# Kernel tuning notes

Hardware: AMD Instinct MI355X
Metric: run time of the kernel (lower is better)

## Reference

```python
import jax, jax.numpy as jnp
import numpy as np

IN_FEATURES = 4096
OUT_FEATURES = 4096
NUM_GROUPS = 32
HARDTANH_MIN = -2.0
HARDTANH_MAX = 2.0
EPS = 1e-6


def setup_inputs() -> dict:
    key = jax.random.key(0)
    k1, k2 = jax.random.split(key)
    x = jax.random.normal(k1, (8192, IN_FEATURES), dtype=jnp.float32)
    W = jax.random.normal(k2, (OUT_FEATURES, IN_FEATURES), dtype=jnp.float32)
    b = jnp.zeros((OUT_FEATURES,), dtype=jnp.float32)
    return {"x": x, "W": W, "b": b}


def reference(x, W, b):
    B = x.shape[0]
    group_size = OUT_FEATURES // NUM_GROUPS
    # GEMM: y[b, n] = sum_k x[b, k] * W[n, k]
    y = jnp.einsum("bk,nk->bn", x, W)
    # GroupNorm over each group of channels per row (no affine scale)
    yg = y.reshape(B, NUM_GROUPS, group_size)
    mean = jnp.mean(yg, axis=2, keepdims=True)
    var = jnp.mean((yg - mean) ** 2, axis=2, keepdims=True)
    norm = (yg - mean) / jnp.sqrt(var + EPS)
    norm = norm.reshape(B, OUT_FEATURES) + b[None, :]
    # kernel clamps to [-2, 2], then outer clamp to [hardtanh_min, hardtanh_max]
    out = jnp.clip(norm, -2.0, 2.0)
    out = jnp.clip(out, HARDTANH_MIN, HARDTANH_MAX)
    return out
```

## Files before the change

kernel.cpp:

```cpp
#include <hip/hip_runtime.h>
#include <hip/hip_bf16.h>
#include <stdint.h>

#define M_DIM 8192
#define N_DIM 4096
#define K_DIM 4096
#define BM 256
#define BN 256
#define BK 64
#define NT 64

typedef __attribute__((ext_vector_type(8))) short short8;
typedef __attribute__((ext_vector_type(4))) float f32x4;
typedef unsigned short ushort_t;

#define SBAR()  asm volatile("s_barrier" ::: "memory")
#define LGKM(n) asm volatile("s_waitcnt lgkmcnt(" #n ")" ::: "memory")
#define VM(n)   asm volatile("s_waitcnt vmcnt(" #n ")" ::: "memory")
#define SCHEDB() __builtin_amdgcn_sched_barrier(0)

__device__ __forceinline__ ushort_t f2bf(float f) {
    uint32_t u = __float_as_uint(f);
    uint32_t r = (u + 0x7FFFu + ((u >> 16) & 1u)) >> 16;
    return (ushort_t)r;
}

__global__ void cvt_f32_bf16(const float4* __restrict__ in, ushort* __restrict__ out4, int n4) {
    int i = blockIdx.x * blockDim.x + threadIdx.x;
    if (i < n4) {
        float4 v = in[i];
        ushort_t a = f2bf(v.x), b = f2bf(v.y), c = f2bf(v.z), d = f2bf(v.w);
        uint32_t lo = (uint32_t)a | ((uint32_t)b << 16);
        uint32_t hi = (uint32_t)c | ((uint32_t)d << 16);
        uint2* o = reinterpret_cast<uint2*>(out4);
        o[i] = make_uint2(lo, hi);
    }
}

__device__ __forceinline__ void gload_lds16(const ushort_t* g, void* l) {
    __builtin_amdgcn_global_load_lds(
        (const __attribute__((address_space(1))) unsigned int*)g,
        (__attribute__((address_space(3))) unsigned int*)l,
        16, 0, 0);
}

__global__ __launch_bounds__(256, 1)
void gemm_gn_kernel(const ushort_t* __restrict__ xb,
                    const ushort_t* __restrict__ wb,
                    const float*   __restrict__ bias,
                    float*         __restrict__ out)
{
    __shared__ char pool[131072];

    const int tid = threadIdx.x;
    const int w   = tid >> 6;
    const int l   = tid & 63;
    const int wr  = w >> 1;
    const int wc  = w & 1;
    const int l15 = l & 15;
    const int l4  = l >> 4;

    const int TN = N_DIM / BN;
    int bid = blockIdx.x;
    bid = (bid & 7) * 64 + (bid >> 3);
    const int brow = (bid / TN) * BM;
    const int bcol = (bid % TN) * BN;

    const int srow  = tid >> 3;
    const int sslot = (tid & 7) ^ (srow & 7);
    const ushort_t* gA = xb + (size_t)(brow + srow) * K_DIM + sslot * 8;
    const ushort_t* gB = wb + (size_t)(bcol + srow) * K_DIM + sslot * 8;
    const int wbase = w * 1024;

    auto STAGE_A = [&](int buf, int half, int kt) {
        const ushort_t* s = gA + (size_t)half * 128 * K_DIM + (size_t)kt * 64;
        char* d = pool + buf * 65536 + half * 16384 + wbase;
        gload_lds16(s,                      d);
        gload_lds16(s + (size_t)32 * K_DIM, d + 4096);
        gload_lds16(s + (size_t)64 * K_DIM, d + 8192);
        gload_lds16(s + (size_t)96 * K_DIM, d + 12288);
    };
    auto STAGE_B = [&](int buf, int half, int kt) {
        const ushort_t* s = gB + (size_t)half * 128 * K_DIM + (size_t)kt * 64;
        char* d = pool + buf * 65536 + 32768 + half * 16384 + wbase;
        gload_lds16(s,                      d);
        gload_lds16(s + (size_t)32 * K_DIM, d + 4096);
        gload_lds16(s + (size_t)64 * K_DIM, d + 8192);
        gload_lds16(s + (size_t)96 * K_DIM, d + 12288);
    };

    const int swz = (l15 & 7) << 4;
    const int x0  = (l4 * 16) ^ swz;
    const int x1  = (64 + l4 * 16) ^ swz;
    const int abase = (wr * 128 + l15) * 128;
    const int bbase = (wc * 128 + l15) * 128;

    short8 afL[8], afH[8], bfL[8], bfH[8];

    auto RD_A = [&](short8* dst, const char* Ab, int mi0) {
#pragma unroll
        for (int m = 0; m < 4; ++m) {
            dst[m * 2]     = *(const short8*)(Ab + abase + (mi0 + m) * 2048 + x0);
            dst[m * 2 + 1] = *(const short8*)(Ab + abase + (mi0 + m) * 2048 + x1);
        }
    };
    auto RD_B = [&](short8* dst, const char* Bb, int ni0) {
#pragma unroll
        for (int n = 0; n < 4; ++n) {
            dst[n * 2]     = *(const short8*)(Bb + bbase + (ni0 + n) * 2048 + x0);
            dst[n * 2 + 1] = *(const short8*)(Bb + bbase + (ni0 + n) * 2048 + x1);
        }
    };

    f32x4 acc[8][8];
#pragma unroll
    for (int i = 0; i < 8; ++i)
#pragma unroll
        for (int j = 0; j < 8; ++j) acc[i][j] = (f32x4){0.f, 0.f, 0.f, 0.f};

    auto MM = [&](short8* A, short8* B, int m0, int n0) {
#pragma unroll
        for (int k = 0; k < 2; ++k)
#pragma unroll
            for (int m = 0; m < 4; ++m)
#pragma unroll
                for (int n = 0; n < 4; ++n)
                    acc[m0 + m][n0 + n] = __builtin_amdgcn_mfma_f32_16x16x32_bf16(
                        A[m * 2 + k], B[n * 2 + k], acc[m0 + m][n0 + n], 0, 0, 0);
    };

    STAGE_A(0, 0, 0); STAGE_A(0, 1, 0);
    STAGE_B(0, 0, 0); STAGE_B(0, 1, 0);
    STAGE_B(1, 0, 1); STAGE_B(1, 1, 1);
    VM(8);
    SBAR();
    RD_B(bfL, pool + 32768, 0);
    RD_A(afL, pool, 0);

    for (int T = 0; T < NT; ++T) {
        const int cb = T & 1;
        const char* Ab = pool + cb * 65536;
        const char* Bb = Ab + 32768;
        const char* Abn = pool + (cb ^ 1) * 65536;
        const char* Bbn = Abn + 32768;

        SBAR();
        RD_A(afH, Ab, 4);
        if (T + 1 < NT) STAGE_A(cb ^ 1, 0, T + 1);
        LGKM(8);
        SCHEDB();
        __builtin_amdgcn_s_setprio(1);
        MM(afL, bfL, 0, 0);
        __builtin_amdgcn_s_setprio(0);

        SBAR();
        RD_B(bfH, Bb, 4);
        if (T + 1 < NT) STAGE_A(cb ^ 1, 1, T + 1);
        LGKM(8);
        SCHEDB();
        __builtin_amdgcn_s_setprio(1);
        MM(afH, bfL, 4, 0);
        __builtin_amdgcn_s_setprio(0);

        if (T + 2 < NT) STAGE_B(cb, 0, T + 2);
        LGKM(0);
        if (T < NT - 2) { VM(8); } else { VM(0); }
        SBAR();
        SCHEDB();
        if (T + 1 < NT) RD_B(bfL, Bbn, 0);
        __builtin_amdgcn_s_setprio(1);
        MM(afH, bfH, 4, 4);
        __builtin_amdgcn_s_setprio(0);

        if (T + 2 < NT) STAGE_B(cb, 1, T + 2);
        if (T < NT - 2) { VM(8); } else { VM(0); }
        SBAR();
        __builtin_amdgcn_s_setprio(1);
        MM(afL, bfH, 0, 4);
        __builtin_amdgcn_s_setprio(0);
        if (T + 1 < NT) RD_A(afL, Abn, 0);
    }

    float bv[8];
#pragma unroll
    for (int ni = 0; ni < 8; ++ni)
        bv[ni] = bias[bcol + wc * 128 + ni * 16 + l15];

    const float inv_gs = 1.0f / 128.0f;
#pragma unroll
    for (int mi = 0; mi < 8; ++mi) {
#pragma unroll
        for (int r = 0; r < 4; ++r) {
            float a = 0.f, b = 0.f;
#pragma unroll
            for (int ni = 0; ni < 8; ++ni) {
                float v = acc[mi][ni][r];
                a += v;
                b += v * v;
            }
#pragma unroll
            for (int m = 1; m < 16; m <<= 1) {
                a += __shfl_xor(a, m);
                b += __shfl_xor(b, m);
            }
            float mean = a * inv_gs;
            float var  = b * inv_gs - mean * mean;
            float inv  = rsqrtf(var + 1e-6f);
            int R = wr * 128 + mi * 16 + l4 * 4 + r;
            size_t rowbase = (size_t)(brow + R) * N_DIM + bcol + wc * 128 + l15;
#pragma unroll
            for (int ni = 0; ni < 8; ++ni) {
                float v = (acc[mi][ni][r] - mean) * inv + bv[ni];
                v = fminf(fmaxf(v, -2.0f), 2.0f);
                out[rowbase + ni * 16] = v;
            }
        }
    }
}

extern "C" void kernel_launch(void* const* d_in, const int* in_sizes, int n_in,
                              void* d_out, int out_size, void* d_ws, size_t ws_size,
                              hipStream_t stream) {
    const float* x = (const float*)d_in[0];
    const float* W = (const float*)d_in[1];
    const float* b = (const float*)d_in[2];
    float* out = (float*)d_out;

    ushort_t* xb = (ushort_t*)d_ws;
    ushort_t* wb = xb + (size_t)M_DIM * K_DIM;

    int n4x = M_DIM * K_DIM / 4;
    cvt_f32_bf16<<<(n4x + 255) / 256, 256, 0, stream>>>(
        (const float4*)x, xb, n4x);
    int n4w = N_DIM * K_DIM / 4;
    cvt_f32_bf16<<<(n4w + 255) / 256, 256, 0, stream>>>(
        (const float4*)W, wb, n4w);

    int grid = (M_DIM / BM) * (N_DIM / BN);
    gemm_gn_kernel<<<grid, 256, 0, stream>>>(xb, wb, b, out);
}
```

Baseline: 311.6 us.

## Use 8 waves per block with interleaved wave tiling and LDS group-norm reduction

After: 324.2 us. 1.04x slower.

```diff
diff --git a/kernel.cpp b/kernel.cpp
--- a/kernel.cpp
+++ b/kernel.cpp
@@ -8,7 +8,7 @@
 #define BM 256
 #define BN 256
 #define BK 64
-#define NT 64
+#define NTL 64
 
 typedef __attribute__((ext_vector_type(8))) short short8;
 typedef __attribute__((ext_vector_type(4))) float f32x4;
@@ -44,7 +44,7 @@
         16, 0, 0);
 }
 
-__global__ __launch_bounds__(256, 1)
+__global__ __launch_bounds__(512, 2)
 void gemm_gn_kernel(const ushort_t* __restrict__ xb,
                     const ushort_t* __restrict__ wb,
                     const float*   __restrict__ bias,
@@ -55,8 +55,8 @@
     const int tid = threadIdx.x;
     const int w   = tid >> 6;
     const int l   = tid & 63;
-    const int wr  = w >> 1;
-    const int wc  = w & 1;
+    const int wr  = w >> 2;
+    const int wc  = w & 3;
     const int l15 = l & 15;
     const int l4  = l >> 4;
 
@@ -66,57 +66,54 @@
     const int brow = (bid / TN) * BM;
     const int bcol = (bid % TN) * BN;
 
-    const int srow  = tid >> 3;
-    const int sslot = (tid & 7) ^ (srow & 7);
-    const ushort_t* gA = xb + (size_t)(brow + srow) * K_DIM + sslot * 8;
-    const ushort_t* gB = wb + (size_t)(bcol + srow) * K_DIM + sslot * 8;
-    const int wbase = w * 1024;
+    const int srow8 = tid >> 3;
+    const int sslot = (tid & 7) ^ (srow8 & 7);
+    const ushort_t* gA = xb + (size_t)(brow + srow8) * K_DIM + sslot * 8;
+    const ushort_t* gB = wb + (size_t)(bcol + srow8) * K_DIM + sslot * 8;
+    const size_t ROW64 = (size_t)64 * K_DIM;
+    const int w1024 = w * 1024;
 
     auto STAGE_A = [&](int buf, int half, int kt) {
         const ushort_t* s = gA + (size_t)half * 128 * K_DIM + (size_t)kt * 64;
-        char* d = pool + buf * 65536 + half * 16384 + wbase;
-        gload_lds16(s,                      d);
-        gload_lds16(s + (size_t)32 * K_DIM, d + 4096);
-        gload_lds16(s + (size_t)64 * K_DIM, d + 8192);
-        gload_lds16(s + (size_t)96 * K_DIM, d + 12288);
+        char* d = pool + buf * 65536 + half * 16384 + w1024;
+        gload_lds16(s,         d);
+        gload_lds16(s + ROW64, d + 8192);
     };
     auto STAGE_B = [&](int buf, int half, int kt) {
         const ushort_t* s = gB + (size_t)half * 128 * K_DIM + (size_t)kt * 64;
-        char* d = pool + buf * 65536 + 32768 + half * 16384 + wbase;
-        gload_lds16(s,                      d);
-        gload_lds16(s + (size_t)32 * K_DIM, d + 4096);
-        gload_lds16(s + (size_t)64 * K_DIM, d + 8192);
-        gload_lds16(s + (size_t)96 * K_DIM, d + 12288);
+        char* d = pool + buf * 65536 + 32768 + half * 16384 + w1024;
+        gload_lds16(s,         d);
+        gload_lds16(s + ROW64, d + 8192);
     };
 
     const int swz = (l15 & 7) << 4;
     const int x0  = (l4 * 16) ^ swz;
     const int x1  = (64 + l4 * 16) ^ swz;
-    const int abase = (wr * 128 + l15) * 128;
-    const int bbase = (wc * 128 + l15) * 128;
-
-    short8 afL[8], afH[8], bfL[8], bfH[8];
+
+    short8 afL[8], afH[8], bfL[4], bfH[4];
 
     auto RD_A = [&](short8* dst, const char* Ab, int mi0) {
 #pragma unroll
         for (int m = 0; m < 4; ++m) {
-            dst[m * 2]     = *(const short8*)(Ab + abase + (mi0 + m) * 2048 + x0);
-            dst[m * 2 + 1] = *(const short8*)(Ab + abase + (mi0 + m) * 2048 + x1);
+            const char* p = Ab + ((mi0 + m) * 32 + wr * 16 + l15) * 128;
+            dst[m * 2]     = *(const short8*)(p + x0);
+            dst[m * 2 + 1] = *(const short8*)(p + x1);
         }
     };
     auto RD_B = [&](short8* dst, const char* Bb, int ni0) {
 #pragma unroll
-        for (int n = 0; n < 4; ++n) {
-            dst[n * 2]     = *(const short8*)(Bb + bbase + (ni0 + n) * 2048 + x0);
-            dst[n * 2 + 1] = *(const short8*)(Bb + bbase + (ni0 + n) * 2048 + x1);
-        }
-    };
-
-    f32x4 acc[8][8];
+        for (int n = 0; n < 2; ++n) {
+            const char* p = Bb + ((ni0 + n) * 64 + wc * 16 + l15) * 128;
+            dst[n * 2]     = *(const short8*)(p + x0);
+            dst[n * 2 + 1] = *(const short8*)(p + x1);
+        }
+    };
+
+    f32x4 acc[8][4];
 #pragma unroll
     for (int i = 0; i < 8; ++i)
 #pragma unroll
-        for (int j = 0; j < 8; ++j) acc[i][j] = (f32x4){0.f, 0.f, 0.f, 0.f};
+        for (int j = 0; j < 4; ++j) acc[i][j] = (f32x4){0.f, 0.f, 0.f, 0.f};
 
     auto MM = [&](short8* A, short8* B, int m0, int n0) {
 #pragma unroll
@@ -124,98 +121,114 @@
 #pragma unroll
             for (int m = 0; m < 4; ++m)
 #pragma unroll
-                for (int n = 0; n < 4; ++n)
+                for (int n = 0; n < 2; ++n)
                     acc[m0 + m][n0 + n] = __builtin_amdgcn_mfma_f32_16x16x32_bf16(
                         A[m * 2 + k], B[n * 2 + k], acc[m0 + m][n0 + n], 0, 0, 0);
     };
 
     STAGE_A(0, 0, 0); STAGE_A(0, 1, 0);
     STAGE_B(0, 0, 0); STAGE_B(0, 1, 0);
-    STAGE_B(1, 0, 1); STAGE_B(1, 1, 1);
-    VM(8);
+    STAGE_A(1, 0, 1); STAGE_A(1, 1, 1);
+    STAGE_B(1, 0, 1);
+    VM(6);
     SBAR();
-    RD_B(bfL, pool + 32768, 0);
-    RD_A(afL, pool, 0);
-
-    for (int T = 0; T < NT; ++T) {
-        const int cb = T & 1;
-        const char* Ab = pool + cb * 65536;
+
+#pragma unroll 2
+    for (int T = 0; T < NTL; ++T) {
+        const int c = T & 1;
+        const char* Ab = pool + c * 65536;
         const char* Bb = Ab + 32768;
-        const char* Abn = pool + (cb ^ 1) * 65536;
-        const char* Bbn = Abn + 32768;
-
-        SBAR();
+
+        RD_A(afL, Ab, 0);
+        RD_B(bfL, Bb, 0);
+        if (T + 1 < NTL) STAGE_B(c ^ 1, 1, T + 1);
+        LGKM(8);
+        SBAR(); LGKM(0); SCHEDB();
+        __builtin_amdgcn_s_setprio(1);
+        MM(afL, bfL, 0, 0);
+        __builtin_amdgcn_s_setprio(0);
+        SBAR();
+
         RD_A(afH, Ab, 4);
-        if (T + 1 < NT) STAGE_A(cb ^ 1, 0, T + 1);
-        LGKM(8);
-        SCHEDB();
-        __builtin_amdgcn_s_setprio(1);
-        MM(afL, bfL, 0, 0);
-        __builtin_amdgcn_s_setprio(0);
-
-        SBAR();
-        RD_B(bfH, Bb, 4);
-        if (T + 1 < NT) STAGE_A(cb ^ 1, 1, T + 1);
-        LGKM(8);
-        SCHEDB();
+        if (T + 2 < NTL) STAGE_A(c, 0, T + 2);
+        SBAR(); LGKM(0); SCHEDB();
         __builtin_amdgcn_s_setprio(1);
         MM(afH, bfL, 4, 0);
         __builtin_amdgcn_s_setprio(0);
-
-        if (T + 2 < NT) STAGE_B(cb, 0, T + 2);
-        LGKM(0);
-        if (T < NT - 2) { VM(8); } else { VM(0); }
-        SBAR();
-        SCHEDB();
-        if (T + 1 < NT) RD_B(bfL, Bbn, 0);
-        __builtin_amdgcn_s_setprio(1);
-        MM(afH, bfH, 4, 4);
-        __builtin_amdgcn_s_setprio(0);
-
-        if (T + 2 < NT) STAGE_B(cb, 1, T + 2);
-        if (T < NT - 2) { VM(8); } else { VM(0); }
-        SBAR();
-        __builtin_amdgcn_s_setprio(1);
-        MM(afL, bfH, 0, 4);
-        __builtin_amdgcn_s_setprio(0);
-        if (T + 1 < NT) RD_A(afL, Abn, 0);
+        SBAR();
+
+        RD_B(bfH, Bb, 2);
+        if (T + 2 < NTL) STAGE_A(c, 1, T + 2);
+        SBAR(); LGKM(0); SCHEDB();
+        __builtin_amdgcn_s_setprio(1);
+        MM(afH, bfH, 4, 2);
+        __builtin_amdgcn_s_setprio(0);
+        SBAR();
+
+        if (T + 2 < NTL) STAGE_B(c, 0, T + 2);
+        if (T < NTL - 2) { VM(6); } else { VM(0); }
+        SBAR(); SCHEDB();
+        __builtin_amdgcn_s_setprio(1);
+        MM(afL, bfH, 0, 2);
+        __builtin_amdgcn_s_setprio(0);
+        SBAR();
     }
 
-    float bv[8];
-#pragma unroll
-    for (int ni = 0; ni < 8; ++ni)
-        bv[ni] = bias[bcol + wc * 128 + ni * 16 + l15];
+    float* redS  = (float*)pool;
+    float* redS2 = (float*)(pool + 8192);
+#pragma unroll
+    for (int mi = 0; mi < 8; ++mi)
+#pragma unroll
+        for (int r = 0; r < 4; ++r) {
+            float gl  = acc[mi][0][r] + acc[mi][1][r];
+            float gh  = acc[mi][2][r] + acc[mi][3][r];
+            float gl2 = acc[mi][0][r] * acc[mi][0][r] + acc[mi][1][r] * acc[mi][1][r];
+            float gh2 = acc[mi][2][r] * acc[mi][2][r] + acc[mi][3][r] * acc[mi][3][r];
+#pragma unroll
+            for (int m = 1; m < 16; m <<= 1) {
+                gl  += __shfl_xor(gl,  m);
+                gh  += __shfl_xor(gh,  m);
+                gl2 += __shfl_xor(gl2, m);
+                gh2 += __shfl_xor(gh2, m);
+            }
+            if (l15 == 0) {
+                int R = mi * 32 + wr * 16 + l4 * 4 + r;
+                redS [R * 8 + wc * 2]     = gl;
+                redS [R * 8 + wc * 2 + 1] = gh;
+                redS2[R * 8 + wc * 2]     = gl2;
+                redS2[R * 8 + wc * 2 + 1] = gh2;
+            }
+        }
+    __syncthreads();
+
+    float bv[4];
+#pragma unroll
+    for (int ni = 0; ni < 4; ++ni)
+        bv[ni] = bias[bcol + ni * 64 + wc * 16 + l15];
 
     const float inv_gs = 1.0f / 128.0f;
 #pragma unroll
-    for (int mi = 0; mi < 8; ++mi) {
+    for (int mi = 0; mi < 8; ++mi)
 #pragma unroll
         for (int r = 0; r < 4; ++r) {
-            float a = 0.f, b = 0.f;
-#pragma unroll
-            for (int ni = 0; ni < 8; ++ni) {
-                float v = acc[mi][ni][r];
-                a += v;
-                b += v * v;
-            }
-#pragma unroll
-            for (int m = 1; m < 16; m <<= 1) {
-                a += __shfl_xor(a, m);
-                b += __shfl_xor(b, m);
-            }
-            float mean = a * inv_gs;
-            float var  = b * inv_gs - mean * mean;
-            float inv  = rsqrtf(var + 1e-6f);
-            int R = wr * 128 + mi * 16 + l4 * 4 + r;
-            size_t rowbase = (size_t)(brow + R) * N_DIM + bcol + wc * 128 + l15;
-#pragma unroll
-            for (int ni = 0; ni < 8; ++ni) {
+            int R = mi * 32 + wr * 16 + l4 * 4 + r;
+            float S0 = redS [R * 8 + 0] + redS [R * 8 + 2] + redS [R * 8 + 4] + redS [R * 8 + 6];
+            float S1 = redS [R * 8 + 1] + redS [R * 8 + 3] + redS [R * 8 + 5] + redS [R * 8 + 7];
+            float T0 = redS2[R * 8 + 0] + redS2[R * 8 + 2] + redS2[R * 8 + 4] + redS2[R * 8 + 6];
+            float T1 = redS2[R * 8 + 1] + redS2[R * 8 + 3] + redS2[R * 8 + 5] + redS2[R * 8 + 7];
+            float mean0 = S0 * inv_gs, mean1 = S1 * inv_gs;
+            float inv0 = rsqrtf(T0 * inv_gs - mean0 * mean0 + 1e-6f);
+            float inv1 = rsqrtf(T1 * inv_gs - mean1 * mean1 + 1e-6f);
+            size_t rowbase = (size_t)(brow + R) * N_DIM + bcol + wc * 16 + l15;
+#pragma unroll
+            for (int ni = 0; ni < 4; ++ni) {
+                float mean = (ni < 2) ? mean0 : mean1;
+                float inv  = (ni < 2) ? inv0  : inv1;
                 float v = (acc[mi][ni][r] - mean) * inv + bv[ni];
                 v = fminf(fmaxf(v, -2.0f), 2.0f);
-                out[rowbase + ni * 16] = v;
+                out[rowbase + ni * 64] = v;
             }
         }
-    }
 }
 
 extern "C" void kernel_launch(void* const* d_in, const int* in_sizes, int n_in,
@@ -237,5 +250,5 @@
         (const float4*)W, wb, n4w);
 
     int grid = (M_DIM / BM) * (N_DIM / BN);
-    gemm_gn_kernel<<<grid, 256, 0, stream>>>(xb, wb, b, out);
-}
+    gemm_gn_kernel<<<grid, 512, 0, stream>>>(xb, wb, b, out);
+}
```
